# Kernel tuning notes

Hardware: AMD Instinct MI355X
Metric: run time of the kernel (lower is better)

## Reference

```python
import jax, jax.numpy as jnp
import numpy as np

B, S, D, H = 8, 256, 16, 256
NH, DH, L = 8, H // 8, 3
H2, H4, FF = H // 2, H // 4, 2 * H


def _ln(x, g, b, eps=1e-5):
    m = jnp.mean(x, axis=-1, keepdims=True)
    v = jnp.var(x, axis=-1, keepdims=True)
    return (x - m) / jnp.sqrt(v + eps) * g + b


def setup_inputs() -> dict:
    key = jax.random.key(0)
    ks = iter(jax.random.split(key, 32))
    w = lambda *sh: jax.random.normal(next(ks), sh, jnp.float32) * 0.05
    inp = {
        'parts': jax.random.normal(next(ks), (B, S, D), jnp.float32),
        'target_sequence': jax.random.randint(next(ks), (B, S), 0, S),
        # part encoder
        'W_pe1': w(H2, D), 'b_pe1': jnp.zeros((H2,)),
        'W_pe2': w(H2, H2), 'b_pe2': jnp.zeros((H2,)),
        'pos_emb': w(S, H4),
        # transformer encoder (3 layers, stacked)
        'Wqkv': w(L, 3 * H, H), 'bqkv': jnp.zeros((L, 3 * H)),
        'Wo': w(L, H, H), 'bo': jnp.zeros((L, H)),
        'ln1_g': jnp.ones((L, H)), 'ln1_b': jnp.zeros((L, H)),
        'W1f': w(L, FF, H), 'b1f': jnp.zeros((L, FF)),
        'W2f': w(L, H, FF), 'b2f': jnp.zeros((L, H)),
        'ln2_g': jnp.ones((L, H)), 'ln2_b': jnp.zeros((L, H)),
        # LSTM decoder
        'Wih': w(4 * H, H), 'Whh': w(4 * H, H),
        'bih': jnp.zeros((4 * H,)), 'bhh': jnp.zeros((4 * H,)),
        # pointer
        'Wp': w(H, H), 'bp': jnp.zeros((H,)), 'v_ptr': w(H),
    }
    return inp


def reference(parts, target_sequence, W_pe1, b_pe1, W_pe2, b_pe2, pos_emb,
              Wqkv, bqkv, Wo, bo, ln1_g, ln1_b, W1f, b1f, W2f, b2f, ln2_g, ln2_b,
              Wih, Whh, bih, bhh, Wp, bp, v_ptr):
    Bk, Sk = parts.shape[:2]
    # ---- encode_inputs (dropout inactive in eval) ----
    pe = jax.nn.relu(parts @ W_pe1.T + b_pe1) @ W_pe2.T + b_pe2          # [B,S,H/2]
    pos = jnp.broadcast_to(pos_emb[None, :Sk], (Bk, Sk, H4))              # [B,S,H/4]
    pad = jnp.zeros((Bk, Sk, H - H2 - H4), parts.dtype)
    x = jnp.concatenate([pe, pos, pad], axis=-1)                          # [B,S,H]
    scale = 1.0 / np.sqrt(DH)
    for l in range(L):  # post-norm transformer encoder layers
        qkv = x @ Wqkv[l].T + bqkv[l]
        q, k, v = jnp.split(qkv, 3, axis=-1)
        q = q.reshape(Bk, Sk, NH, DH)
        k = k.reshape(Bk, Sk, NH, DH)
        v = v.reshape(Bk, Sk, NH, DH)
        att = jax.nn.softmax(jnp.einsum('bqhd,bkhd->bhqk', q, k) * scale, axis=-1)
        o = jnp.einsum('bhqk,bkhd->bqhd', att, v).reshape(Bk, Sk, H)
        o = o @ Wo[l].T + bo[l]
        x = _ln(x + o, ln1_g[l], ln1_b[l])
        f = jax.nn.relu(x @ W1f[l].T + b1f[l]) @ W2f[l].T + b2f[l]
        x = _ln(x + f, ln2_g[l], ln2_b[l])
    enc = x                                                               # [B,S,H]
    # ---- teacher-forced LSTM decode (teacher_forcing_ratio=1.0) ----
    gathered = jnp.take_along_axis(enc, target_sequence[:, :, None], axis=1)  # [B,T,H]
    dec_in = jnp.concatenate([jnp.zeros((Bk, 1, H), enc.dtype), gathered[:, :-1]], 1)
    dec_in = dec_in.transpose(1, 0, 2)                                    # [T,B,H]

    def step(carry, xt):
        h, c = carry
        g = xt @ Wih.T + bih + h @ Whh.T + bhh
        i, f, gg, o = jnp.split(g, 4, axis=-1)
        c = jax.nn.sigmoid(f) * c + jax.nn.sigmoid(i) * jnp.tanh(gg)
        h = jax.nn.sigmoid(o) * jnp.tanh(c)
        return (h, c), h

    h0 = jnp.zeros((Bk, H), enc.dtype)
    _, dec_out = jax.lax.scan(step, (h0, h0), dec_in)
    dec_out = dec_out.transpose(1, 0, 2)                                  # [B,T,H]
    # ---- pointer logits: v . tanh(Wp d_t + Wp e_i), batched over (t,i) ----
    pd = dec_out @ Wp.T + bp                                              # [B,T,H]
    pen = enc @ Wp.T + bp                                                 # [B,S,H]
    logits = jnp.tanh(pd[:, :, None, :] + pen[:, None, :, :]) @ v_ptr     # [B,T,S]
    return logits
```

## Files before the change

kernel.cpp:

```cpp
#include <hip/hip_runtime.h>
#include <cstdint>
#include <cstddef>

typedef _Float16 h2 __attribute__((ext_vector_type(2)));
typedef short bf16x8 __attribute__((ext_vector_type(8)));
typedef float f32x4 __attribute__((ext_vector_type(4)));

__device__ __forceinline__ float sigf(float x) { return 1.0f / (1.0f + __expf(-x)); }
__device__ __forceinline__ float tanhfast(float x) {
  float e = __expf(-2.0f * fabsf(x));
  float t = (1.0f - e) / (1.0f + e);
  return copysignf(t, x);
}
__device__ __forceinline__ h2 cvt2(float a, float b) {
  h2 r; r.x = (_Float16)a; r.y = (_Float16)b; return r;
}
__device__ __forceinline__ h2 bch2(unsigned int u) { return __builtin_bit_cast(h2, u); }
__device__ __forceinline__ unsigned int bcu(h2 v) { return __builtin_bit_cast(unsigned int, v); }
__device__ __forceinline__ unsigned short f2bf(float f) {
  unsigned int u = __float_as_uint(f);
  u = (u + 0x7fffu + ((u >> 16) & 1u)) >> 16;
  return (unsigned short)u;
}

__device__ __forceinline__ float fdot2f(h2 a, h2 b, float c) {
#if __has_builtin(__builtin_amdgcn_fdot2)
  return __builtin_amdgcn_fdot2(a, b, c, false);
#else
  return fmaf((float)a.x, (float)b.x, fmaf((float)a.y, (float)b.y, c));
#endif
}

__global__ void convert_bf(const float* __restrict__ src, ushort* __restrict__ dst, int n) {
  int i = blockIdx.x * 256 + threadIdx.x;
  if (i < n) dst[i] = f2bf(src[i]);
}

__global__ void part_encoder(const float* __restrict__ parts, const float* __restrict__ Wpe1,
                             const float* __restrict__ bpe1, const float* __restrict__ Wpe2,
                             const float* __restrict__ bpe2, const float* __restrict__ pos,
                             float* __restrict__ x, ushort* __restrict__ xb) {
  __shared__ float prow[16];
  __shared__ float pe1[128];
  int row = blockIdx.x;
  int s = row & 255;
  int tid = threadIdx.x;
  if (tid < 16) prow[tid] = parts[row * 16 + tid];
  __syncthreads();
  float a = bpe1[tid];
#pragma unroll
  for (int k = 0; k < 16; ++k) a = fmaf(prow[k], Wpe1[tid * 16 + k], a);
  pe1[tid] = fmaxf(a, 0.0f);
  __syncthreads();
  float a2 = bpe2[tid];
  for (int k = 0; k < 128; ++k) a2 = fmaf(pe1[k], Wpe2[tid * 128 + k], a2);
  x[(size_t)row * 256 + tid] = a2;
  xb[(size_t)row * 256 + tid] = f2bf(a2);
  if (tid < 64) {
    float p = pos[s * 64 + tid];
    x[(size_t)row * 256 + 128 + tid] = p;
    xb[(size_t)row * 256 + 128 + tid] = f2bf(p);
    x[(size_t)row * 256 + 192 + tid] = 0.0f;
    xb[(size_t)row * 256 + 192 + tid] = 0;
  }
}

template <int ACT, int OUTBF>
__global__ __launch_bounds__(256) void gemm_bf16(
    const ushort* __restrict__ A, const ushort* __restrict__ Wt,
    const float* __restrict__ bias1, const float* __restrict__ bias2,
    void* __restrict__ Cout, int N, int K) {
  int wid = threadIdx.x >> 6;
  int lane = threadIdx.x & 63;
  int m0 = blockIdx.y * 64 + wid * 16;
  int n0 = blockIdx.x * 64;
  int r15 = lane & 15;
  int kg = lane >> 4;
  f32x4 acc0 = {0.f, 0.f, 0.f, 0.f}, acc1 = acc0, acc2 = acc0, acc3 = acc0;
  const ushort* arow = A + (size_t)(m0 + r15) * K + kg * 8;
  const ushort* w0 = Wt + (size_t)(n0 + r15) * K + kg * 8;
  const ushort* w1 = w0 + (size_t)16 * K;
  const ushort* w2 = w0 + (size_t)32 * K;
  const ushort* w3 = w0 + (size_t)48 * K;
  for (int k0 = 0; k0 < K; k0 += 32) {
    bf16x8 af = *(const bf16x8*)(arow + k0);
    bf16x8 b0 = *(const bf16x8*)(w0 + k0);
    bf16x8 b1 = *(const bf16x8*)(w1 + k0);
    bf16x8 b2 = *(const bf16x8*)(w2 + k0);
    bf16x8 b3 = *(const bf16x8*)(w3 + k0);
    acc0 = __builtin_amdgcn_mfma_f32_16x16x32_bf16(af, b0, acc0, 0, 0, 0);
    acc1 = __builtin_amdgcn_mfma_f32_16x16x32_bf16(af, b1, acc1, 0, 0, 0);
    acc2 = __builtin_amdgcn_mfma_f32_16x16x32_bf16(af, b2, acc2, 0, 0, 0);
    acc3 = __builtin_amdgcn_mfma_f32_16x16x32_bf16(af, b3, acc3, 0, 0, 0);
  }
#pragma unroll
  for (int nn = 0; nn < 4; ++nn) {
    f32x4 a = (nn == 0) ? acc0 : (nn == 1) ? acc1 : (nn == 2) ? acc2 : acc3;
    int n = n0 + nn * 16 + r15;
    float bsum = bias1[n] + (bias2 ? bias2[n] : 0.0f);
#pragma unroll
    for (int r = 0; r < 4; ++r) {
      int m = m0 + kg * 4 + r;
      float v = a[r] + bsum;
      if (ACT == 1) v = fmaxf(v, 0.0f);
      if (OUTBF == 1)
        ((ushort*)Cout)[(size_t)m * N + n] = f2bf(v);
      else
        ((float*)Cout)[(size_t)m * N + n] = v;
    }
  }
}

__global__ void attn_kernel(const float* __restrict__ qkv, ushort* __restrict__ attout) {
  extern __shared__ float sm[];
  float* kl = sm;
  float* ql = sm + 256 * 33;
  float* sc = sm + 256 * 33 + 32 * 33;
  int qt = blockIdx.x, h = blockIdx.y, b = blockIdx.z;
  int tid = threadIdx.x;
  {
    int j = tid;
    const float* src = qkv + (size_t)(b * 256 + j) * 768 + 256 + h * 32;
#pragma unroll
    for (int d = 0; d < 32; d += 4) {
      float4 v = *(const float4*)(src + d);
      kl[j * 33 + d] = v.x; kl[j * 33 + d + 1] = v.y; kl[j * 33 + d + 2] = v.z; kl[j * 33 + d + 3] = v.w;
    }
  }
  {
    int i = tid >> 3, d4 = (tid & 7) * 4;
    const float* src = qkv + (size_t)(b * 256 + qt * 32 + i) * 768 + h * 32;
    float4 v = *(const float4*)(src + d4);
    ql[i * 33 + d4] = v.x; ql[i * 33 + d4 + 1] = v.y; ql[i * 33 + d4 + 2] = v.z; ql[i * 33 + d4 + 3] = v.w;
  }
  __syncthreads();
  int i = tid >> 3, c = tid & 7;
  const float scale = 0.17677669529663687f;
  float sv[32];
  float mx = -1e30f;
  for (int jj = 0; jj < 32; ++jj) {
    int j = jj * 8 + c;
    float s = 0.0f;
#pragma unroll
    for (int d = 0; d < 32; ++d) s = fmaf(ql[i * 33 + d], kl[j * 33 + d], s);
    s *= scale;
    sv[jj] = s;
    mx = fmaxf(mx, s);
  }
  mx = fmaxf(mx, __shfl_xor(mx, 1));
  mx = fmaxf(mx, __shfl_xor(mx, 2));
  mx = fmaxf(mx, __shfl_xor(mx, 4));
  float sum = 0.0f;
  for (int jj = 0; jj < 32; ++jj) {
    float p = __expf(sv[jj] - mx);
    sc[i * 257 + jj * 8 + c] = p;
    sum += p;
  }
  sum += __shfl_xor(sum, 1);
  sum += __shfl_xor(sum, 2);
  sum += __shfl_xor(sum, 4);
  float inv = 1.0f / sum;
  __syncthreads();
  float a0 = 0, a1 = 0, a2 = 0, a3 = 0;
  int d0 = c * 4;
  const float* vbase = qkv + 512 + h * 32 + d0;
  for (int j = 0; j < 256; ++j) {
    float p = sc[i * 257 + j];
    float4 v = *(const float4*)(vbase + (size_t)(b * 256 + j) * 768);
    a0 = fmaf(p, v.x, a0); a1 = fmaf(p, v.y, a1); a2 = fmaf(p, v.z, a2); a3 = fmaf(p, v.w, a3);
  }
  int orow = b * 256 + qt * 32 + i;
  ushort4 o4;
  o4.x = f2bf(a0 * inv); o4.y = f2bf(a1 * inv); o4.z = f2bf(a2 * inv); o4.w = f2bf(a3 * inv);
  *(ushort4*)&attout[(size_t)orow * 256 + h * 32 + d0] = o4;
}

__global__ void ln_residual(float* __restrict__ x, const float* __restrict__ o,
                            const float* __restrict__ g, const float* __restrict__ bt,
                            ushort* __restrict__ xb) {
  int row = blockIdx.x, tid = threadIdx.x;
  float e = x[(size_t)row * 256 + tid] + o[(size_t)row * 256 + tid];
  float s = e, q = e * e;
#pragma unroll
  for (int off = 32; off >= 1; off >>= 1) {
    s += __shfl_xor(s, off);
    q += __shfl_xor(q, off);
  }
  __shared__ float ps[4], pq[4];
  int wid = tid >> 6, lane = tid & 63;
  if (lane == 0) { ps[wid] = s; pq[wid] = q; }
  __syncthreads();
  float St = ps[0] + ps[1] + ps[2] + ps[3];
  float Qt = pq[0] + pq[1] + pq[2] + pq[3];
  float mean = St * (1.0f / 256.0f);
  float var = Qt * (1.0f / 256.0f) - mean * mean;
  float y = (e - mean) * rsqrtf(var + 1e-5f) * g[tid] + bt[tid];
  x[(size_t)row * 256 + tid] = y;
  xb[(size_t)row * 256 + tid] = f2bf(y);
}

__global__ void gather_dec_in(const ushort* __restrict__ encb, const int* __restrict__ ts,
                              ushort* __restrict__ dec_in) {
  int bx = blockIdx.x;
  int t = bx >> 3, b = bx & 7;
  int tid = threadIdx.x;
  ushort4 v = {0, 0, 0, 0};
  if (t > 0) {
    int sidx = ts[b * 256 + t - 1];
    v = *(const ushort4*)&encb[((size_t)(b * 256 + sidx)) * 256 + tid * 4];
  }
  *(ushort4*)&dec_in[(size_t)bx * 256 + tid * 4] = v;
}

__global__ __attribute__((amdgpu_flat_work_group_size(512, 512), amdgpu_waves_per_eu(1, 1)))
void lstm_scan(const float* __restrict__ Xw, const float* __restrict__ Whh,
               ushort* __restrict__ dec_out) {
  extern __shared__ char smem[];
  uint4* wlds = (uint4*)smem;
  h2* hbuf = (h2*)(smem + 131072);
  int b = blockIdx.x;
  int t0 = threadIdx.x;
  int u = t0 >> 1, p = t0 & 1;
  int rA = u + 256 * p;
  int rB = u + 512 + 256 * p;

  h2 w0[96], w1[96];
  {
    const float4* sA = (const float4*)(Whh + (size_t)rA * 256);
    const float4* sB = (const float4*)(Whh + (size_t)rB * 256);
#pragma unroll
    for (int k = 0; k < 48; ++k) {
      float4 v = sA[k];
      w0[2 * k] = cvt2(v.x, v.y);
      w0[2 * k + 1] = cvt2(v.z, v.w);
    }
#pragma unroll
    for (int k = 0; k < 48; ++k) {
      float4 v = sB[k];
      w1[2 * k] = cvt2(v.x, v.y);
      w1[2 * k + 1] = cvt2(v.z, v.w);
    }
#pragma unroll
    for (int qc = 0; qc < 8; ++qc) {
      float4 vA0 = sA[48 + 2 * qc], vA1 = sA[48 + 2 * qc + 1];
      float4 vB0 = sB[48 + 2 * qc], vB1 = sB[48 + 2 * qc + 1];
      uint4 uA, uB;
      uA.x = bcu(cvt2(vA0.x, vA0.y)); uA.y = bcu(cvt2(vA0.z, vA0.w));
      uA.z = bcu(cvt2(vA1.x, vA1.y)); uA.w = bcu(cvt2(vA1.z, vA1.w));
      uB.x = bcu(cvt2(vB0.x, vB0.y)); uB.y = bcu(cvt2(vB0.z, vB0.w));
      uB.z = bcu(cvt2(vB1.x, vB1.y)); uB.w = bcu(cvt2(vB1.z, vB1.w));
      wlds[qc * 1024 + rA] = uA;
      wlds[qc * 1024 + rB] = uB;
    }
  }
  if (t0 < 128) ((uint4*)hbuf)[t0 & 63] = make_uint4(0, 0, 0, 0);
  float c = 0.0f;
  float xnA = Xw[(size_t)b * 1024 + rA];
  float xnB = Xw[(size_t)b * 1024 + rB];
  __syncthreads();

  for (int t = 0; t < 256; ++t) {
    float xwA = xnA, xwB = xnB;
    if (t < 255) {
      const float* xp = Xw + (size_t)((t + 1) * 8 + b) * 1024;
      xnA = xp[rA]; xnB = xp[rB];
    }
    const uint4* hb = (const uint4*)(hbuf + (size_t)(t & 1) * 128);
    float a0 = 0.0f, a1 = 0.0f;
#pragma unroll
    for (int q = 0; q < 24; ++q) {
      uint4 hv = hb[q];
      h2 hx = bch2(hv.x), hy = bch2(hv.y), hz = bch2(hv.z), hw = bch2(hv.w);
      a0 = fdot2f(w0[4 * q], hx, a0); a0 = fdot2f(w0[4 * q + 1], hy, a0);
      a0 = fdot2f(w0[4 * q + 2], hz, a0); a0 = fdot2f(w0[4 * q + 3], hw, a0);
      a1 = fdot2f(w1[4 * q], hx, a1); a1 = fdot2f(w1[4 * q + 1], hy, a1);
      a1 = fdot2f(w1[4 * q + 2], hz, a1); a1 = fdot2f(w1[4 * q + 3], hw, a1);
    }
#pragma unroll
    for (int qc = 0; qc < 8; ++qc) {
      uint4 hv = hb[24 + qc];
      h2 hx = bch2(hv.x), hy = bch2(hv.y), hz = bch2(hv.z), hw = bch2(hv.w);
      uint4 uA = wlds[qc * 1024 + rA];
      uint4 uB = wlds[qc * 1024 + rB];
      a0 = fdot2f(bch2(uA.x), hx, a0); a0 = fdot2f(bch2(uA.y), hy, a0);
      a0 = fdot2f(bch2(uA.z), hz, a0); a0 = fdot2f(bch2(uA.w), hw, a0);
      a1 = fdot2f(bch2(uB.x), hx, a1); a1 = fdot2f(bch2(uB.y), hy, a1);
      a1 = fdot2f(bch2(uB.z), hz, a1); a1 = fdot2f(bch2(uB.w), hw, a1);
    }
    a0 += xwA;
    a1 += xwB;
    float ev = sigf(a0) * tanhfast(a1);
    float ep = __shfl_xor(ev, 1);
    if (p == 1) {
      c = sigf(a0) * c + ep;
      float hv_ = sigf(a1) * tanhfast(c);
      ((_Float16*)(hbuf + (size_t)((t + 1) & 1) * 128))[u] = (_Float16)hv_;
      dec_out[((size_t)(b * 256 + t)) * 256 + u] = f2bf(hv_);
    }
    __syncthreads();
  }
}

__global__ void transpose_pen(const float* __restrict__ pen, float* __restrict__ penT) {
  int bx = blockIdx.x;
  int b = bx >> 8, h = bx & 255;
  int i = threadIdx.x;
  penT[(size_t)bx * 256 + i] = pen[((size_t)(b * 256 + i)) * 256 + h];
}

__global__ void pointer_kernel(const float* __restrict__ pd, const float* __restrict__ penT,
                               const float* __restrict__ vptr, float* __restrict__ out) {
  __shared__ float pdr[256];
  __shared__ float vl[256];
  int bx = blockIdx.x;
  int b = bx >> 8;
  int tid = threadIdx.x;
  pdr[tid] = pd[(size_t)bx * 256 + tid];
  vl[tid] = vptr[tid];
  __syncthreads();
  const float* pT = penT + (size_t)b * 256 * 256;
  float acc = 0.0f;
  for (int h = 0; h < 256; ++h) {
    acc = fmaf(vl[h], tanhfast(pdr[h] + pT[(size_t)h * 256 + tid]), acc);
  }
  out[(size_t)bx * 256 + tid] = acc;
}

extern "C" void kernel_launch(void* const* d_in, const int* in_sizes, int n_in,
                              void* d_out, int out_size, void* d_ws, size_t ws_size,
                              hipStream_t stream) {
  const float* parts = (const float*)d_in[0];
  const int* ts = (const int*)d_in[1];
  const float* Wpe1 = (const float*)d_in[2];
  const float* bpe1 = (const float*)d_in[3];
  const float* Wpe2 = (const float*)d_in[4];
  const float* bpe2 = (const float*)d_in[5];
  const float* pos = (const float*)d_in[6];
  const float* Wqkv = (const float*)d_in[7];
  const float* bqkv = (const float*)d_in[8];
  const float* Wo = (const float*)d_in[9];
  const float* bo = (const float*)d_in[10];
  const float* ln1g = (const float*)d_in[11];
  const float* ln1b = (const float*)d_in[12];
  const float* W1f = (const float*)d_in[13];
  const float* b1f = (const float*)d_in[14];
  const float* W2f = (const float*)d_in[15];
  const float* b2f = (const float*)d_in[16];
  const float* ln2g = (const float*)d_in[17];
  const float* ln2b = (const float*)d_in[18];
  const float* Wih = (const float*)d_in[19];
  const float* Whh = (const float*)d_in[20];
  const float* bih = (const float*)d_in[21];
  const float* bhh = (const float*)d_in[22];
  const float* Wp = (const float*)d_in[23];
  const float* bp = (const float*)d_in[24];
  const float* vptr = (const float*)d_in[25];
  float* out = (float*)d_out;

  float* W = (float*)d_ws;
  float* xbuf = W;
  ushort* xbf = (ushort*)(W + 524288);
  float* SCR = W + 786432;
  float* qkvb = SCR;
  float* obuf = SCR + 1572864;
  float* Xw = SCR;
  float* pdb = SCR;
  float* penb = SCR + 524288;
  float* penTb = SCR + 1048576;
  ushort* attbf = (ushort*)(W + 2883584);
  ushort* ffbf = (ushort*)(W + 3145728);
  ushort* dec_inbf = (ushort*)(W + 3145728);
  ushort* dec_outbf = (ushort*)(W + 3407872);
  ushort* wqkvbf = (ushort*)(W + 3670016);
  ushort* wobf   = (ushort*)(W + 3964928);
  ushort* w1fbf  = (ushort*)(W + 4063232);
  ushort* w2fbf  = (ushort*)(W + 4259840);
  ushort* wihbf  = (ushort*)(W + 4456448);
  ushort* wpbf   = (ushort*)(W + 4587520);

  const int attnLDS = (256 * 33 + 32 * 33 + 32 * 257) * 4;
  const int scanLDS = 131072 + 1024;
  hipFuncSetAttribute((const void*)attn_kernel, hipFuncAttributeMaxDynamicSharedMemorySize, attnLDS);
  hipFuncSetAttribute((const void*)lstm_scan, hipFuncAttributeMaxDynamicSharedMemorySize, scanLDS);

  convert_bf<<<(589824 + 255) / 256, 256, 0, stream>>>(Wqkv, wqkvbf, 589824);
  convert_bf<<<(196608 + 255) / 256, 256, 0, stream>>>(Wo, wobf, 196608);
  convert_bf<<<(393216 + 255) / 256, 256, 0, stream>>>(W1f, w1fbf, 393216);
  convert_bf<<<(393216 + 255) / 256, 256, 0, stream>>>(W2f, w2fbf, 393216);
  convert_bf<<<(262144 + 255) / 256, 256, 0, stream>>>(Wih, wihbf, 262144);
  convert_bf<<<(65536 + 255) / 256, 256, 0, stream>>>(Wp, wpbf, 65536);

  part_encoder<<<2048, 128, 0, stream>>>(parts, Wpe1, bpe1, Wpe2, bpe2, pos, xbuf, xbf);
  for (int l = 0; l < 3; ++l) {
    gemm_bf16<0, 0><<<dim3(12, 32), 256, 0, stream>>>(xbf, wqkvbf + (size_t)l * 196608,
                                                      bqkv + l * 768, nullptr, qkvb, 768, 256);
    attn_kernel<<<dim3(8, 8, 8), 256, attnLDS, stream>>>(qkvb, attbf);
    gemm_bf16<0, 0><<<dim3(4, 32), 256, 0, stream>>>(attbf, wobf + (size_t)l * 65536,
                                                     bo + l * 256, nullptr, obuf, 256, 256);
    ln_residual<<<2048, 256, 0, stream>>>(xbuf, obuf, ln1g + l * 256, ln1b + l * 256, xbf);
    gemm_bf16<1, 1><<<dim3(8, 32), 256, 0, stream>>>(xbf, w1fbf + (size_t)l * 131072,
                                                     b1f + l * 512, nullptr, ffbf, 512, 256);
    gemm_bf16<0, 0><<<dim3(4, 32), 256, 0, stream>>>(ffbf, w2fbf + (size_t)l * 131072,
                                                     b2f + l * 256, nullptr, obuf, 256, 512);
    ln_residual<<<2048, 256, 0, stream>>>(xbuf, obuf, ln2g + l * 256, ln2b + l * 256, xbf);
  }
  gather_dec_in<<<2048, 64, 0, stream>>>(xbf, ts, dec_inbf);
  gemm_bf16<0, 0><<<dim3(16, 32), 256, 0, stream>>>(dec_inbf, wihbf, bih, bhh, Xw, 1024, 256);
  lstm_scan<<<8, 512, scanLDS, stream>>>(Xw, Whh, dec_outbf);
  gemm_bf16<0, 0><<<dim3(4, 32), 256, 0, stream>>>(dec_outbf, wpbf, bp, nullptr, pdb, 256, 256);
  gemm_bf16<0, 0><<<dim3(4, 32), 256, 0, stream>>>(xbf, wpbf, bp, nullptr, penb, 256, 256);
  transpose_pen<<<2048, 256, 0, stream>>>(penb, penTb);
  pointer_kernel<<<2048, 256, 0, stream>>>(pdb, penTb, vptr, out);
}
```

Before: 863.2 us.

## Fuse weight conversions, shrink GEMM blocks to one wave, write pen transposed

The six weight-conversion launches are merged into one kernel that dispatches by index range. The bf16 GEMM now runs one 64-thread wave per block covering 16 rows, giving four times as many blocks for better CU occupancy on these small GEMMs. A new output mode writes the pen projection straight into transposed layout with float4 stores, which removes the separate transpose kernel and its buffer. The trade-off is more block scheduling overhead and strided transposed writes.

```diff
diff --git a/kernel.cpp b/kernel.cpp
--- a/kernel.cpp
+++ b/kernel.cpp
@@ -1,6 +1,7 @@
 #include <hip/hip_runtime.h>
 #include <cstdint>
 #include <cstddef>
+
 
 typedef _Float16 h2 __attribute__((ext_vector_type(2)));
 typedef short bf16x8 __attribute__((ext_vector_type(8)));
@@ -31,9 +32,24 @@
 #endif
 }
 
-__global__ void convert_bf(const float* __restrict__ src, ushort* __restrict__ dst, int n) {
+__global__ void convert_all(const float* __restrict__ s0, ushort* __restrict__ d0,
+                            const float* __restrict__ s1, ushort* __restrict__ d1,
+                            const float* __restrict__ s2, ushort* __restrict__ d2,
+                            const float* __restrict__ s3, ushort* __restrict__ d3,
+                            const float* __restrict__ s4, ushort* __restrict__ d4,
+                            const float* __restrict__ s5, ushort* __restrict__ d5) {
   int i = blockIdx.x * 256 + threadIdx.x;
-  if (i < n) dst[i] = f2bf(src[i]);
+  if (i < 589824) { d0[i] = f2bf(s0[i]); return; }
+  i -= 589824;
+  if (i < 196608) { d1[i] = f2bf(s1[i]); return; }
+  i -= 196608;
+  if (i < 393216) { d2[i] = f2bf(s2[i]); return; }
+  i -= 393216;
+  if (i < 393216) { d3[i] = f2bf(s3[i]); return; }
+  i -= 393216;
+  if (i < 262144) { d4[i] = f2bf(s4[i]); return; }
+  i -= 262144;
+  if (i < 65536) d5[i] = f2bf(s5[i]);
 }
 
 __global__ void part_encoder(const float* __restrict__ parts, const float* __restrict__ Wpe1,
@@ -65,14 +81,13 @@
   }
 }
 
-template <int ACT, int OUTBF>
-__global__ __launch_bounds__(256) void gemm_bf16(
+template <int ACT, int OUT>
+__global__ __launch_bounds__(64) void gemm_bf16(
     const ushort* __restrict__ A, const ushort* __restrict__ Wt,
     const float* __restrict__ bias1, const float* __restrict__ bias2,
     void* __restrict__ Cout, int N, int K) {
-  int wid = threadIdx.x >> 6;
-  int lane = threadIdx.x & 63;
-  int m0 = blockIdx.y * 64 + wid * 16;
+  int lane = threadIdx.x;
+  int m0 = blockIdx.y * 16;
   int n0 = blockIdx.x * 64;
   int r15 = lane & 15;
   int kg = lane >> 4;
@@ -98,15 +113,22 @@
     f32x4 a = (nn == 0) ? acc0 : (nn == 1) ? acc1 : (nn == 2) ? acc2 : acc3;
     int n = n0 + nn * 16 + r15;
     float bsum = bias1[n] + (bias2 ? bias2[n] : 0.0f);
-#pragma unroll
-    for (int r = 0; r < 4; ++r) {
-      int m = m0 + kg * 4 + r;
-      float v = a[r] + bsum;
-      if (ACT == 1) v = fmaxf(v, 0.0f);
-      if (OUTBF == 1)
-        ((ushort*)Cout)[(size_t)m * N + n] = f2bf(v);
-      else
-        ((float*)Cout)[(size_t)m * N + n] = v;
+    if (OUT == 3) {
+      int b = m0 >> 8;
+      int mloc = (m0 & 255) + kg * 4;
+      float4 o4 = {a[0] + bsum, a[1] + bsum, a[2] + bsum, a[3] + bsum};
+      *(float4*)&((float*)Cout)[((size_t)(b * 256 + n)) * 256 + mloc] = o4;
+    } else {
+#pragma unroll
+      for (int r = 0; r < 4; ++r) {
+        int m = m0 + kg * 4 + r;
+        float v = a[r] + bsum;
+        if (ACT == 1) v = fmaxf(v, 0.0f);
+        if (OUT == 1)
+          ((ushort*)Cout)[(size_t)m * N + n] = f2bf(v);
+        else
+          ((float*)Cout)[(size_t)m * N + n] = v;
+      }
     }
   }
 }
@@ -213,8 +235,8 @@
 }
 
 __global__ __attribute__((amdgpu_flat_work_group_size(512, 512), amdgpu_waves_per_eu(1, 1)))
-void lstm_scan(const float* __restrict__ Xw, const float* __restrict__ Whh,
-               ushort* __restrict__ dec_out) {
+void lstm_scan512(const float* __restrict__ Xw, const float* __restrict__ Whh,
+                  ushort* __restrict__ dec_out) {
   extern __shared__ char smem[];
   uint4* wlds = (uint4*)smem;
   h2* hbuf = (h2*)(smem + 131072);
@@ -299,13 +321,6 @@
     }
     __syncthreads();
   }
-}
-
-__global__ void transpose_pen(const float* __restrict__ pen, float* __restrict__ penT) {
-  int bx = blockIdx.x;
-  int b = bx >> 8, h = bx & 255;
-  int i = threadIdx.x;
-  penT[(size_t)bx * 256 + i] = pen[((size_t)(b * 256 + i)) * 256 + h];
 }
 
 __global__ void pointer_kernel(const float* __restrict__ pd, const float* __restrict__ penT,
@@ -365,7 +380,6 @@
   float* obuf = SCR + 1572864;
   float* Xw = SCR;
   float* pdb = SCR;
-  float* penb = SCR + 524288;
   float* penTb = SCR + 1048576;
   ushort* attbf = (ushort*)(W + 2883584);
   ushort* ffbf = (ushort*)(W + 3145728);
@@ -379,36 +393,31 @@
   ushort* wpbf   = (ushort*)(W + 4587520);
 
   const int attnLDS = (256 * 33 + 32 * 33 + 32 * 257) * 4;
-  const int scanLDS = 131072 + 1024;
+  const int scan512LDS = 131072 + 1024;
   hipFuncSetAttribute((const void*)attn_kernel, hipFuncAttributeMaxDynamicSharedMemorySize, attnLDS);
-  hipFuncSetAttribute((const void*)lstm_scan, hipFuncAttributeMaxDynamicSharedMemorySize, scanLDS);
-
-  convert_bf<<<(589824 + 255) / 256, 256, 0, stream>>>(Wqkv, wqkvbf, 589824);
-  convert_bf<<<(196608 + 255) / 256, 256, 0, stream>>>(Wo, wobf, 196608);
-  convert_bf<<<(393216 + 255) / 256, 256, 0, stream>>>(W1f, w1fbf, 393216);
-  convert_bf<<<(393216 + 255) / 256, 256, 0, stream>>>(W2f, w2fbf, 393216);
-  convert_bf<<<(262144 + 255) / 256, 256, 0, stream>>>(Wih, wihbf, 262144);
-  convert_bf<<<(65536 + 255) / 256, 256, 0, stream>>>(Wp, wpbf, 65536);
+  hipFuncSetAttribute((const void*)lstm_scan512, hipFuncAttributeMaxDynamicSharedMemorySize, scan512LDS);
+
+  convert_all<<<7424, 256, 0, stream>>>(Wqkv, wqkvbf, Wo, wobf, W1f, w1fbf,
+                                        W2f, w2fbf, Wih, wihbf, Wp, wpbf);
 
   part_encoder<<<2048, 128, 0, stream>>>(parts, Wpe1, bpe1, Wpe2, bpe2, pos, xbuf, xbf);
   for (int l = 0; l < 3; ++l) {
-    gemm_bf16<0, 0><<<dim3(12, 32), 256, 0, stream>>>(xbf, wqkvbf + (size_t)l * 196608,
+    gemm_bf16<0, 0><<<dim3(12, 128), 64, 0, stream>>>(xbf, wqkvbf + (size_t)l * 196608,
                                                       bqkv + l * 768, nullptr, qkvb, 768, 256);
     attn_kernel<<<dim3(8, 8, 8), 256, attnLDS, stream>>>(qkvb, attbf);
-    gemm_bf16<0, 0><<<dim3(4, 32), 256, 0, stream>>>(attbf, wobf + (size_t)l * 65536,
+    gemm_bf16<0, 0><<<dim3(4, 128), 64, 0, stream>>>(attbf, wobf + (size_t)l * 65536,
                                                      bo + l * 256, nullptr, obuf, 256, 256);
     ln_residual<<<2048, 256, 0, stream>>>(xbuf, obuf, ln1g + l * 256, ln1b + l * 256, xbf);
-    gemm_bf16<1, 1><<<dim3(8, 32), 256, 0, stream>>>(xbf, w1fbf + (size_t)l * 131072,
+    gemm_bf16<1, 1><<<dim3(8, 128), 64, 0, stream>>>(xbf, w1fbf + (size_t)l * 131072,
                                                      b1f + l * 512, nullptr, ffbf, 512, 256);
-    gemm_bf16<0, 0><<<dim3(4, 32), 256, 0, stream>>>(ffbf, w2fbf + (size_t)l * 131072,
+    gemm_bf16<0, 0><<<dim3(4, 128), 64, 0, stream>>>(ffbf, w2fbf + (size_t)l * 131072,
                                                      b2f + l * 256, nullptr, obuf, 256, 512);
     ln_residual<<<2048, 256, 0, stream>>>(xbuf, obuf, ln2g + l * 256, ln2b + l * 256, xbf);
   }
   gather_dec_in<<<2048, 64, 0, stream>>>(xbf, ts, dec_inbf);
-  gemm_bf16<0, 0><<<dim3(16, 32), 256, 0, stream>>>(dec_inbf, wihbf, bih, bhh, Xw, 1024, 256);
-  lstm_scan<<<8, 512, scanLDS, stream>>>(Xw, Whh, dec_outbf);
-  gemm_bf16<0, 0><<<dim3(4, 32), 256, 0, stream>>>(dec_outbf, wpbf, bp, nullptr, pdb, 256, 256);
-  gemm_bf16<0, 0><<<dim3(4, 32), 256, 0, stream>>>(xbf, wpbf, bp, nullptr, penb, 256, 256);
-  transpose_pen<<<2048, 256, 0, stream>>>(penb, penTb);
+  gemm_bf16<0, 0><<<dim3(16, 128), 64, 0, stream>>>(dec_inbf, wihbf, bih, bhh, Xw, 1024, 256);
+  lstm_scan512<<<8, 512, scan512LDS, stream>>>(Xw, Whh, dec_outbf);
+  gemm_bf16<0, 0><<<dim3(4, 128), 64, 0, stream>>>(dec_outbf, wpbf, bp, nullptr, pdb, 256, 256);
+  gemm_bf16<0, 3><<<dim3(4, 128), 64, 0, stream>>>(xbf, wpbf, bp, nullptr, penTb, 256, 256);
   pointer_kernel<<<2048, 256, 0, stream>>>(pdb, penTb, vptr, out);
 }
```

New measurement: 825.5 us. 4.4% less time.
